# Kernel tuning notes

Hardware: AMD Instinct MI355X
Metric: run time of the kernel (lower is better)

The kernel has to match this reference:

```python
import jax, jax.numpy as jnp
import numpy as np

TEMPERATURE = 0.5
EPS_NORM = 1e-12   # F.normalize eps
EPS_DEN = 1e-8     # denominator clamp


def setup_inputs() -> dict:
    key = jax.random.key(0)
    k1, k2 = jax.random.split(key)
    B, D = 4096, 256
    return {
        "proj_feat1": jax.random.normal(k1, (B, D), dtype=jnp.float32),
        "proj_feat2": jax.random.normal(k2, (B, D), dtype=jnp.float32),
    }


def _l2_normalize(x):
    n = jnp.sqrt(jnp.sum(x * x, axis=1, keepdims=True))
    return x / jnp.maximum(n, EPS_NORM)


def reference(proj_feat1, proj_feat2):
    B = proj_feat1.shape[0]
    z1 = _l2_normalize(proj_feat1)
    z2 = _l2_normalize(proj_feat2)
    z = jnp.concatenate([z1, z2], axis=0)          # [2B, D], unit rows
    # cosine similarity of unit-norm rows == plain matmul (GEMM instead of
    # the O(N^2*D) broadcasted intermediate in the torch source)
    sim = jnp.matmul(z, z.T)                        # [2B, 2B]
    s = jnp.exp(sim / TEMPERATURE)                  # [2B, 2B]
    idx = jnp.arange(2 * B)
    pos_idx = (idx + B) % (2 * B)                   # roll(eye, B, dim=1) positions
    numerator = s[idx, pos_idx]                     # [2B]
    # negatives: everything except the diagonal
    diag = jnp.diagonal(s)
    denominator = jnp.sum(s, axis=1) - diag         # sum * (1 - eye)
    denominator = jnp.maximum(denominator, EPS_DEN)
    loss = jnp.mean(-jnp.log(numerator / denominator))
    return loss
```

## Files before the change

kernel.cpp:

```cpp
#include <hip/hip_runtime.h>
#include <hip/hip_bf16.h>

#define NTOT 8192
#define BB   4096
#define DD   256

typedef __attribute__((ext_vector_type(8))) short short8v;
typedef __attribute__((ext_vector_type(4))) float f32x4;

__device__ __forceinline__ int swz(int off) { return off ^ (((off >> 9) & 7) << 4); }

__device__ __forceinline__ unsigned short f2bf(float f) {
    __hip_bfloat16 h = __float2bfloat16(f);
    union { __hip_bfloat16 h; unsigned short u; } cv;
    cv.h = h;
    return cv.u;
}

__global__ __launch_bounds__(256) void k_normalize(
    const float* __restrict__ x1, const float* __restrict__ x2,
    unsigned short* __restrict__ zbf,
    float* __restrict__ selfdot, float* __restrict__ posdot)
{
    const int lane = threadIdx.x & 63;
    const int pair = blockIdx.x * 4 + (threadIdx.x >> 6);

    const float4 a = *(const float4*)(x1 + (size_t)pair * DD + lane * 4);
    const float4 b = *(const float4*)(x2 + (size_t)pair * DD + lane * 4);

    float s1 = a.x * a.x + a.y * a.y + a.z * a.z + a.w * a.w;
    float s2 = b.x * b.x + b.y * b.y + b.z * b.z + b.w * b.w;
#pragma unroll
    for (int off = 1; off < 64; off <<= 1) {
        s1 += __shfl_xor(s1, off);
        s2 += __shfl_xor(s2, off);
    }
    const float inv1 = 1.0f / fmaxf(sqrtf(s1), 1e-12f);
    const float inv2 = 1.0f / fmaxf(sqrtf(s2), 1e-12f);

    const float4 z1 = make_float4(a.x * inv1, a.y * inv1, a.z * inv1, a.w * inv1);
    const float4 z2 = make_float4(b.x * inv2, b.y * inv2, b.z * inv2, b.w * inv2);

    float sd1 = z1.x * z1.x + z1.y * z1.y + z1.z * z1.z + z1.w * z1.w;
    float sd2 = z2.x * z2.x + z2.y * z2.y + z2.z * z2.z + z2.w * z2.w;
    float pd  = z1.x * z2.x + z1.y * z2.y + z1.z * z2.z + z1.w * z2.w;
#pragma unroll
    for (int off = 1; off < 64; off <<= 1) {
        sd1 += __shfl_xor(sd1, off);
        sd2 += __shfl_xor(sd2, off);
        pd  += __shfl_xor(pd, off);
    }

    ushort4 u1, u2;
    u1.x = f2bf(z1.x); u1.y = f2bf(z1.y); u1.z = f2bf(z1.z); u1.w = f2bf(z1.w);
    u2.x = f2bf(z2.x); u2.y = f2bf(z2.y); u2.z = f2bf(z2.z); u2.w = f2bf(z2.w);
    *(ushort4*)(zbf + (size_t)pair * DD + lane * 4) = u1;
    *(ushort4*)(zbf + (size_t)(pair + BB) * DD + lane * 4) = u2;

    if (lane == 0) {
        selfdot[pair] = sd1;
        selfdot[pair + BB] = sd2;
        posdot[pair] = pd;
        posdot[pair + BB] = pd;
    }
}

__global__ __launch_bounds__(256, 2) void k_simsum(
    const unsigned short* __restrict__ zbf, float* __restrict__ S_part)
{
    __shared__ unsigned short Bsh[32 * DD];

    const int tid  = threadIdx.x;
    const int lane = tid & 63;
    const int wave = tid >> 6;
    const int frow = lane & 15;
    const int kgrp = (lane >> 4) * 8;
    const int row0 = blockIdx.x * 256 + wave * 64;
    const int colBase = blockIdx.y * 512;

    short8v Afrag[4][8];
#pragma unroll
    for (int rt = 0; rt < 4; ++rt) {
        const int row = row0 + rt * 16 + frow;
#pragma unroll
        for (int kk = 0; kk < 8; ++kk)
            Afrag[rt][kk] = *(const short8v*)(zbf + (size_t)row * DD + kk * 32 + kgrp);
    }

    float rs[4][4];
#pragma unroll
    for (int rt = 0; rt < 4; ++rt)
#pragma unroll
        for (int q = 0; q < 4; ++q) rs[rt][q] = 0.0f;

    for (int t = 0; t < 16; ++t) {
        __syncthreads();
        {
            const uint4* src = (const uint4*)(zbf + (size_t)(colBase + t * 32) * DD);
#pragma unroll
            for (int i = 0; i < 4; ++i) {
                const int q = tid + i * 256;
                *(uint4*)((char*)Bsh + swz(q * 16)) = src[q];
            }
        }
        __syncthreads();

        f32x4 acc[4][2];
#pragma unroll
        for (int rt = 0; rt < 4; ++rt) {
#pragma unroll
            for (int c = 0; c < 2; ++c) {
                acc[rt][c][0] = 0.0f; acc[rt][c][1] = 0.0f;
                acc[rt][c][2] = 0.0f; acc[rt][c][3] = 0.0f;
            }
        }

#pragma unroll
        for (int kk = 0; kk < 8; ++kk) {
            const int kbyte = (kk * 32 + kgrp) * 2;
            const short8v b0 = *(const short8v*)((const char*)Bsh + swz(frow * 512 + kbyte));
            const short8v b1 = *(const short8v*)((const char*)Bsh + swz((16 + frow) * 512 + kbyte));
#pragma unroll
            for (int rt = 0; rt < 4; ++rt) {
                acc[rt][0] = __builtin_amdgcn_mfma_f32_16x16x32_bf16(Afrag[rt][kk], b0, acc[rt][0], 0, 0, 0);
                acc[rt][1] = __builtin_amdgcn_mfma_f32_16x16x32_bf16(Afrag[rt][kk], b1, acc[rt][1], 0, 0, 0);
            }
        }

#pragma unroll
        for (int rt = 0; rt < 4; ++rt)
#pragma unroll
            for (int q = 0; q < 4; ++q)
                rs[rt][q] += __expf(2.0f * acc[rt][0][q]) + __expf(2.0f * acc[rt][1][q]);
    }

#pragma unroll
    for (int rt = 0; rt < 4; ++rt) {
#pragma unroll
        for (int q = 0; q < 4; ++q) {
            float v = rs[rt][q];
            v += __shfl_xor(v, 1);
            v += __shfl_xor(v, 2);
            v += __shfl_xor(v, 4);
            v += __shfl_xor(v, 8);
            if (frow == 0) {
                const int row = row0 + rt * 16 + (lane >> 4) * 4 + q;
                S_part[blockIdx.y * NTOT + row] = v;
            }
        }
    }
}

__global__ __launch_bounds__(256) void k_final(
    const float* __restrict__ S_part, const float* __restrict__ selfdot,
    const float* __restrict__ posdot, float* __restrict__ out)
{
    __shared__ float red[4];
    const int tid = threadIdx.x;
    float acc = 0.0f;
    for (int i = tid; i < NTOT; i += 256) {
        float s = 0.0f;
#pragma unroll
        for (int sp = 0; sp < 16; ++sp) s += S_part[sp * NTOT + i];
        const float den = fmaxf(s - expf(2.0f * selfdot[i]), 1e-8f);
        acc += logf(den) - 2.0f * posdot[i];
    }
#pragma unroll
    for (int off = 1; off < 64; off <<= 1) acc += __shfl_xor(acc, off);
    if ((tid & 63) == 0) red[tid >> 6] = acc;
    __syncthreads();
    if (tid == 0) out[0] = (red[0] + red[1] + red[2] + red[3]) * (1.0f / (float)NTOT);
}

extern "C" void kernel_launch(void* const* d_in, const int* in_sizes, int n_in,
                              void* d_out, int out_size, void* d_ws, size_t ws_size,
                              hipStream_t stream) {
    const float* x1 = (const float*)d_in[0];
    const float* x2 = (const float*)d_in[1];
    float* out = (float*)d_out;

    char* ws = (char*)d_ws;
    unsigned short* zbf = (unsigned short*)ws;
    size_t off = (size_t)NTOT * DD * sizeof(unsigned short);
    float* S_part = (float*)(ws + off);
    off += (size_t)16 * NTOT * sizeof(float);
    float* selfdot = (float*)(ws + off);
    off += (size_t)NTOT * sizeof(float);
    float* posdot = (float*)(ws + off);

    k_normalize<<<dim3(BB / 4), dim3(256), 0, stream>>>(x1, x2, zbf, selfdot, posdot);
    k_simsum<<<dim3(32, 16), dim3(256), 0, stream>>>(zbf, S_part);
    k_final<<<dim3(1), dim3(256), 0, stream>>>(S_part, selfdot, posdot, out);
}
```

Measured before the change: 117.5 us.

## Double-buffer B tiles via direct global-to-LDS loads and parallelize final reduction

The similarity-sum kernel now stages 64-row B tiles into two LDS buffers with global_load_lds, prefetching the next tile while MFMAs run on the current one. This halves the barrier count and hides global load latency. The exp is rewritten as exp2f with a folded constant. The final reduction moves from one block to 32 blocks that combine through atomicAdd, with an extra launch to zero the output first, so the summation order is no longer fixed and the result can vary slightly from run to run.

```diff
diff --git a/kernel.cpp b/kernel.cpp
--- a/kernel.cpp
+++ b/kernel.cpp
@@ -8,12 +8,9 @@
 typedef __attribute__((ext_vector_type(8))) short short8v;
 typedef __attribute__((ext_vector_type(4))) float f32x4;
 
-__device__ __forceinline__ int swz(int off) { return off ^ (((off >> 9) & 7) << 4); }
-
 __device__ __forceinline__ unsigned short f2bf(float f) {
-    __hip_bfloat16 h = __float2bfloat16(f);
     union { __hip_bfloat16 h; unsigned short u; } cv;
-    cv.h = h;
+    cv.h = __float2bfloat16(f);
     return cv.u;
 }
 
@@ -68,24 +65,31 @@
 __global__ __launch_bounds__(256, 2) void k_simsum(
     const unsigned short* __restrict__ zbf, float* __restrict__ S_part)
 {
-    __shared__ unsigned short Bsh[32 * DD];
+    __shared__ char Bsh[2][32768];
 
     const int tid  = threadIdx.x;
     const int lane = tid & 63;
     const int wave = tid >> 6;
     const int frow = lane & 15;
-    const int kgrp = (lane >> 4) * 8;
     const int row0 = blockIdx.x * 256 + wave * 64;
-    const int colBase = blockIdx.y * 512;
+    const int colStart = blockIdx.y * 512;
 
     short8v Afrag[4][8];
 #pragma unroll
     for (int rt = 0; rt < 4; ++rt) {
         const int row = row0 + rt * 16 + frow;
+        const unsigned short* ap = zbf + (size_t)row * DD + (lane >> 4) * 8;
 #pragma unroll
         for (int kk = 0; kk < 8; ++kk)
-            Afrag[rt][kk] = *(const short8v*)(zbf + (size_t)row * DD + kk * 32 + kgrp);
-    }
+            Afrag[rt][kk] = *(const short8v*)(ap + kk * 32);
+    }
+
+    const int jswz = (tid & 31) ^ ((tid >> 5) & 7);
+    const char* gsrc0 = (const char*)zbf + (size_t)colStart * 512
+                        + (tid >> 5) * 512 + jswz * 16;
+
+    const int base0 = frow * 512 + (lane >> 4) * 16;
+    const int bmask = (frow & 7) << 4;
 
     float rs[4][4];
 #pragma unroll
@@ -93,45 +97,63 @@
 #pragma unroll
         for (int q = 0; q < 4; ++q) rs[rt][q] = 0.0f;
 
-    for (int t = 0; t < 16; ++t) {
+#pragma unroll
+    for (int r = 0; r < 8; ++r)
+        __builtin_amdgcn_global_load_lds(
+            (const __attribute__((address_space(1))) unsigned int*)(gsrc0 + r * 4096),
+            (__attribute__((address_space(3))) unsigned int*)(&Bsh[0][0] + tid * 16 + r * 4096),
+            16, 0, 0);
+    __syncthreads();
+
+    int cur = 0;
+    for (int t = 0; t < 8; ++t) {
+        if (t < 7) {
+            const char* gs = gsrc0 + (size_t)(t + 1) * 32768;
+            char* ld = &Bsh[cur ^ 1][0] + tid * 16;
+#pragma unroll
+            for (int r = 0; r < 8; ++r)
+                __builtin_amdgcn_global_load_lds(
+                    (const __attribute__((address_space(1))) unsigned int*)(gs + r * 4096),
+                    (__attribute__((address_space(3))) unsigned int*)(ld + r * 4096),
+                    16, 0, 0);
+        }
+
+#pragma unroll
+        for (int c2 = 0; c2 < 2; ++c2) {
+            f32x4 acc[4][2];
+#pragma unroll
+            for (int rt = 0; rt < 4; ++rt)
+#pragma unroll
+                for (int c = 0; c < 2; ++c) {
+                    acc[rt][c][0] = 0.0f; acc[rt][c][1] = 0.0f;
+                    acc[rt][c][2] = 0.0f; acc[rt][c][3] = 0.0f;
+                }
+
+#pragma unroll
+            for (int kk = 0; kk < 8; ++kk) {
+                const char* bp = &Bsh[cur][0] + ((base0 + kk * 64) ^ bmask)
+                                 + c2 * 16384;
+                short8v b0 = *(const short8v*)(bp);
+                short8v b1 = *(const short8v*)(bp + 8192);
+#pragma unroll
+                for (int rt = 0; rt < 4; ++rt) {
+                    acc[rt][0] = __builtin_amdgcn_mfma_f32_16x16x32_bf16(
+                        Afrag[rt][kk], b0, acc[rt][0], 0, 0, 0);
+                    acc[rt][1] = __builtin_amdgcn_mfma_f32_16x16x32_bf16(
+                        Afrag[rt][kk], b1, acc[rt][1], 0, 0, 0);
+                }
+            }
+
+#pragma unroll
+            for (int rt = 0; rt < 4; ++rt)
+#pragma unroll
+                for (int q = 0; q < 4; ++q)
+                    rs[rt][q] += exp2f(acc[rt][0][q] * 2.8853900817779268f)
+                               + exp2f(acc[rt][1][q] * 2.8853900817779268f);
+        }
+
         __syncthreads();
-        {
-            const uint4* src = (const uint4*)(zbf + (size_t)(colBase + t * 32) * DD);
-#pragma unroll
-            for (int i = 0; i < 4; ++i) {
-                const int q = tid + i * 256;
-                *(uint4*)((char*)Bsh + swz(q * 16)) = src[q];
-            }
-        }
-        __syncthreads();
-
-        f32x4 acc[4][2];
-#pragma unroll
-        for (int rt = 0; rt < 4; ++rt) {
-#pragma unroll
-            for (int c = 0; c < 2; ++c) {
-                acc[rt][c][0] = 0.0f; acc[rt][c][1] = 0.0f;
-                acc[rt][c][2] = 0.0f; acc[rt][c][3] = 0.0f;
-            }
-        }
-
-#pragma unroll
-        for (int kk = 0; kk < 8; ++kk) {
-            const int kbyte = (kk * 32 + kgrp) * 2;
-            const short8v b0 = *(const short8v*)((const char*)Bsh + swz(frow * 512 + kbyte));
-            const short8v b1 = *(const short8v*)((const char*)Bsh + swz((16 + frow) * 512 + kbyte));
-#pragma unroll
-            for (int rt = 0; rt < 4; ++rt) {
-                acc[rt][0] = __builtin_amdgcn_mfma_f32_16x16x32_bf16(Afrag[rt][kk], b0, acc[rt][0], 0, 0, 0);
-                acc[rt][1] = __builtin_amdgcn_mfma_f32_16x16x32_bf16(Afrag[rt][kk], b1, acc[rt][1], 0, 0, 0);
-            }
-        }
-
-#pragma unroll
-        for (int rt = 0; rt < 4; ++rt)
-#pragma unroll
-            for (int q = 0; q < 4; ++q)
-                rs[rt][q] += __expf(2.0f * acc[rt][0][q]) + __expf(2.0f * acc[rt][1][q]);
+        cur ^= 1;
     }
 
 #pragma unroll
@@ -151,25 +173,26 @@
     }
 }
 
+__global__ void k_zero(float* out) { out[0] = 0.0f; }
+
 __global__ __launch_bounds__(256) void k_final(
     const float* __restrict__ S_part, const float* __restrict__ selfdot,
     const float* __restrict__ posdot, float* __restrict__ out)
 {
     __shared__ float red[4];
     const int tid = threadIdx.x;
-    float acc = 0.0f;
-    for (int i = tid; i < NTOT; i += 256) {
-        float s = 0.0f;
-#pragma unroll
-        for (int sp = 0; sp < 16; ++sp) s += S_part[sp * NTOT + i];
-        const float den = fmaxf(s - expf(2.0f * selfdot[i]), 1e-8f);
-        acc += logf(den) - 2.0f * posdot[i];
-    }
+    const int i = blockIdx.x * 256 + tid;
+    float s = 0.0f;
+#pragma unroll
+    for (int sp = 0; sp < 16; ++sp) s += S_part[sp * NTOT + i];
+    const float den = fmaxf(s - expf(2.0f * selfdot[i]), 1e-8f);
+    float acc = logf(den) - 2.0f * posdot[i];
 #pragma unroll
     for (int off = 1; off < 64; off <<= 1) acc += __shfl_xor(acc, off);
     if ((tid & 63) == 0) red[tid >> 6] = acc;
     __syncthreads();
-    if (tid == 0) out[0] = (red[0] + red[1] + red[2] + red[3]) * (1.0f / (float)NTOT);
+    if (tid == 0)
+        atomicAdd(out, (red[0] + red[1] + red[2] + red[3]) * (1.0f / (float)NTOT));
 }
 
 extern "C" void kernel_launch(void* const* d_in, const int* in_sizes, int n_in,
@@ -190,5 +213,6 @@
 
     k_normalize<<<dim3(BB / 4), dim3(256), 0, stream>>>(x1, x2, zbf, selfdot, posdot);
     k_simsum<<<dim3(32, 16), dim3(256), 0, stream>>>(zbf, S_part);
-    k_final<<<dim3(1), dim3(256), 0, stream>>>(S_part, selfdot, posdot, out);
-}
+    k_zero<<<dim3(1), dim3(1), 0, stream>>>(out);
+    k_final<<<dim3(32), dim3(256), 0, stream>>>(S_part, selfdot, posdot, out);
+}
```

Result: faster. 110.0 us (-6.4%).
